# Kernel tuning notes

Hardware: AMD Instinct MI355X
Metric: run time of the kernel (lower is better)

## Reference

```python
import jax, jax.numpy as jnp
import numpy as np

DEPTH, DIM, HEADS, DH, MLP, N, B = 6, 192, 12, 16, 768, 256, 32
INNER = HEADS * DH  # 192


def setup_inputs() -> dict:
    key = jax.random.key(0)
    ks = jax.random.split(key, 10)
    w = lambda i, shape: jax.random.normal(ks[i], shape, dtype=jnp.float32) * 0.02
    return {
        'x': jax.random.normal(ks[0], (B, N, DIM), dtype=jnp.float32),
        'ln1_g': jnp.ones((DEPTH, DIM), jnp.float32),
        'ln1_b': jnp.zeros((DEPTH, DIM), jnp.float32),
        'Wq': w(1, (DEPTH, DIM, INNER)),
        'Wkv': w(2, (DEPTH, DIM, 2 * INNER)),
        'lsa_scale': jnp.full((DEPTH, HEADS), DH ** -0.5, dtype=jnp.float32),
        'mix_pre': jax.random.normal(ks[3], (DEPTH, HEADS, HEADS), dtype=jnp.float32),
        'mix_post': jax.random.normal(ks[4], (DEPTH, HEADS, HEADS), dtype=jnp.float32),
        'Wo': w(5, (DEPTH, INNER, DIM)),
        'bo': jnp.zeros((DEPTH, DIM), jnp.float32),
        'ls1': jnp.full((DEPTH, DIM), 0.1, dtype=jnp.float32),
        'ln2_g': jnp.ones((DEPTH, DIM), jnp.float32),
        'ln2_b': jnp.zeros((DEPTH, DIM), jnp.float32),
        'W1': w(6, (DEPTH, DIM, MLP)),
        'b1': jnp.zeros((DEPTH, MLP), jnp.float32),
        'W2': w(7, (DEPTH, MLP, DIM)),
        'b2': jnp.zeros((DEPTH, DIM), jnp.float32),
        'ls2': jnp.full((DEPTH, DIM), 0.1, dtype=jnp.float32),
    }


def _ln(x, g, b, eps=1e-5):
    m = x.mean(-1, keepdims=True)
    v = ((x - m) ** 2).mean(-1, keepdims=True)
    return (x - m) * jax.lax.rsqrt(v + eps) * g + b


def _heads(t, b, n):
    # (b, n, h*d) -> (b, h, n, d)
    return t.reshape(b, n, HEADS, DH).transpose(0, 2, 1, 3)


def _forward(x, ln1_g, ln1_b, Wq, Wkv, lsa_scale, mix_pre, mix_post, Wo, bo,
             ls1, ln2_g, ln2_b, W1, b1, W2, b2, ls2):
    b, n, _ = x.shape
    diag = jnp.arange(n)
    for l in range(DEPTH):
        # --- PreNorm + talking-heads LSA attention + LayerScale(0.1) ---
        h = _ln(x, ln1_g[l], ln1_b[l])
        q = _heads(h @ Wq[l], b, n)
        k, v = jnp.split(h @ Wkv[l], 2, axis=-1)
        k, v = _heads(k, b, n), _heads(v, b, n)
        dots = jnp.einsum('bhid,bhjd->bhij', q, k) * lsa_scale[l][None, :, None, None]
        # LSA: source sets diagonal to -1e-09 (literal, near-zero) when if_patch_attn
        dots = dots.at[:, :, diag, diag].set(-1e-9)
        dots = jnp.einsum('bhij,hg->bgij', dots, mix_pre[l])
        a = jax.nn.softmax(dots, axis=-1)
        a = jnp.einsum('bhij,hg->bgij', a, mix_post[l])
        o = jnp.einsum('bhij,bhjd->bhid', a, v)
        o = o.transpose(0, 2, 1, 3).reshape(b, n, INNER) @ Wo[l] + bo[l]
        x = x + o * ls1[l]
        # --- PreNorm + GELU FFN + LayerScale(0.1) ---
        h2 = _ln(x, ln2_g[l], ln2_b[l])
        f = jax.nn.gelu(h2 @ W1[l] + b1[l], approximate=False) @ W2[l] + b2[l]
        x = x + f * ls2[l]
    return x


def reference(x, ln1_g, ln1_b, Wq, Wkv, lsa_scale, mix_pre, mix_post, Wo, bo,
              ls1, ln2_g, ln2_b, W1, b1, W2, b2, ls2):
    return _forward(x, ln1_g, ln1_b, Wq, Wkv, lsa_scale, mix_pre, mix_post, Wo,
                    bo, ls1, ln2_g, ln2_b, W1, b1, W2, b2, ls2)
```

## Files before the change

kernel.cpp:

```cpp
#include <hip/hip_runtime.h>
#include <hip/hip_bf16.h>

#define DEPTH   6
#define DIM     192
#define HEADS   12
#define DH      16
#define MLPD    768
#define SEQ     256
#define BATCH   32
#define ROWS    (BATCH*SEQ)

typedef __attribute__((ext_vector_type(8))) short short8;
typedef __attribute__((ext_vector_type(4))) float f32x4;
typedef __attribute__((ext_vector_type(4))) _Float16 half4;
typedef __hip_bfloat16 bf16_t;
typedef _Float16 f16_t;

__device__ __forceinline__ bf16_t f2b(float v){ return __float2bfloat16(v); }
__device__ __forceinline__ ushort f2u(float v){
    union{ bf16_t b; ushort u; } w; w.b = __float2bfloat16(v); return w.u;
}
__device__ __forceinline__ f16_t u2h(ushort u){ union{ ushort u; f16_t h; } w; w.u = u; return w.h; }
__device__ __forceinline__ ushort h2u(f16_t h){ union{ ushort u; f16_t h; } w; w.h = h; return w.u; }

__device__ __forceinline__ void async16(ushort* lds, const ushort* gp){
    __builtin_amdgcn_global_load_lds(
        (const __attribute__((address_space(1))) uint*)gp,
        (__attribute__((address_space(3))) uint*)lds, 16, 0, 0);
}

__global__ void copy_kernel(const float* __restrict__ x, float* __restrict__ xr, int n){
    int i = blockIdx.x*256 + threadIdx.x;
    if (i < n) xr[i] = x[i];
}

__device__ __forceinline__ void wt_tile(const float* __restrict__ W,
        ushort* __restrict__ WT, int K, int N, int l, int tx, int ty,
        int tid, ushort* T){
    const float* src = W + ((size_t)l*K + tx*64)*N + ty*64;
    ushort* dst = WT + ((size_t)l*N + ty*64)*K + tx*64;
    int r = tid >> 2, c4 = (tid & 3)*16;
    #pragma unroll
    for (int u=0; u<4; u++){
        float4 v = *(const float4*)(src + (size_t)r*N + c4 + u*4);
        T[(c4+u*4+0)*72 + r] = f2u(v.x);
        T[(c4+u*4+1)*72 + r] = f2u(v.y);
        T[(c4+u*4+2)*72 + r] = f2u(v.z);
        T[(c4+u*4+3)*72 + r] = f2u(v.w);
    }
    __syncthreads();
    int n = tid >> 2, k8 = (tid & 3)*16;
    #pragma unroll
    for (int u=0; u<2; u++)
        *(uint4*)(dst + (size_t)n*K + k8 + u*8) = *(uint4*)&T[n*72 + k8 + u*8];
}

__global__ __launch_bounds__(256) void wt_all(
        const float* __restrict__ Wq, const float* __restrict__ Wkv,
        const float* __restrict__ Wo, const float* __restrict__ W1,
        const float* __restrict__ W2,
        ushort* __restrict__ WqT, ushort* __restrict__ WkvT,
        ushort* __restrict__ WoT, ushort* __restrict__ W1T,
        ushort* __restrict__ W2T){
    __shared__ ushort T[64*72];
    int id = blockIdx.x, l = blockIdx.y, tid = threadIdx.x;
    if (id < 9)       wt_tile(Wq,  WqT,  192, 192, l, id/3,       id%3,       tid, T);
    else if (id < 27) wt_tile(Wkv, WkvT, 192, 384, l, (id-9)/6,   (id-9)%6,   tid, T);
    else if (id < 36) wt_tile(Wo,  WoT,  192, 192, l, (id-27)/3,  (id-27)%3,  tid, T);
    else if (id < 72) wt_tile(W1,  W1T,  192, 768, l, (id-36)/12, (id-36)%12, tid, T);
    else              wt_tile(W2,  W2T,  768, 192, l, (id-72)/3,  (id-72)%3,  tid, T);
}

template<int MODE, int NT>
__global__ __launch_bounds__(256) void gemm_ln_kernel(
        const float* __restrict__ xres, const float* __restrict__ ln_g,
        const float* __restrict__ ln_b, const ushort* __restrict__ BT0,
        const ushort* __restrict__ BT1, const float* __restrict__ bias,
        f16_t* __restrict__ out0, f16_t* __restrict__ out1){
    __shared__ ushort As[64*200];
    __shared__ ushort Bs[2][6*2048];
    int tid = threadIdx.x, lane = tid & 63, w = tid >> 6;
    int bm = blockIdx.x*64;
    int tile0 = blockIdx.y*NT;
    auto issueB = [&](int t, int buf){
        int bn = (tile0 + t)*64;
        const ushort* bt; int bnl;
        if (MODE == 0 && bn >= DIM){ bt = BT1; bnl = bn - DIM; }
        else { bt = BT0; bnl = bn; }
        const ushort* bp = bt + (size_t)(bnl + (tid>>2))*DIM + (tid&3)*8;
        #pragma unroll
        for (int c=0; c<6; c++)
            async16(&Bs[buf][c*2048 + tid*8], bp + c*32);
    };
    issueB(0, 0);
    float g0 = ln_g[lane], g1 = ln_g[lane+64], g2 = ln_g[lane+128];
    float e0 = ln_b[lane], e1 = ln_b[lane+64], e2 = ln_b[lane+128];
    for (int it = 0; it < 16; it++){
        int r = (w<<4) + it;
        const float* xr = xres + (size_t)(bm + r)*DIM;
        float v0 = xr[lane], v1 = xr[lane+64], v2 = xr[lane+128];
        float s = v0+v1+v2;
        #pragma unroll
        for (int off=32; off; off>>=1) s += __shfl_xor(s, off, 64);
        float m = s*(1.0f/192.0f);
        float d0=v0-m, d1=v1-m, d2=v2-m;
        float q = d0*d0+d1*d1+d2*d2;
        #pragma unroll
        for (int off=32; off; off>>=1) q += __shfl_xor(q, off, 64);
        float inv = rsqrtf(q*(1.0f/192.0f) + 1e-5f);
        ushort* dst = &As[r*200];
        dst[lane]     = f2u(d0*inv*g0 + e0);
        dst[lane+64]  = f2u(d1*inv*g1 + e1);
        dst[lane+128] = f2u(d2*inv*g2 + e2);
    }
    __syncthreads();
    int wrow = w >> 1, wcol = w & 1;
    int quad = lane >> 4, mr = lane & 15;
    for (int t = 0; t < NT; t++){
        if (t+1 < NT) issueB(t+1, (t+1)&1);
        const ushort* B = Bs[t&1];
        f32x4 acc[2][2] = {};
        #pragma unroll
        for (int c = 0; c < 6; c++){
            short8 a0 = *(const short8*)&As[(wrow*32+mr)*200    + c*32 + quad*8];
            short8 a1 = *(const short8*)&As[(wrow*32+16+mr)*200 + c*32 + quad*8];
            short8 b0 = *(const short8*)&B[c*2048 + (wcol*32+mr)*32    + quad*8];
            short8 b1 = *(const short8*)&B[c*2048 + (wcol*32+16+mr)*32 + quad*8];
            acc[0][0] = __builtin_amdgcn_mfma_f32_16x16x32_bf16(a0, b0, acc[0][0], 0,0,0);
            acc[0][1] = __builtin_amdgcn_mfma_f32_16x16x32_bf16(a0, b1, acc[0][1], 0,0,0);
            acc[1][0] = __builtin_amdgcn_mfma_f32_16x16x32_bf16(a1, b0, acc[1][0], 0,0,0);
            acc[1][1] = __builtin_amdgcn_mfma_f32_16x16x32_bf16(a1, b1, acc[1][1], 0,0,0);
        }
        int bn = (tile0 + t)*64;
        #pragma unroll
        for (int rr=0; rr<2; rr++){
            #pragma unroll
            for (int cc=0; cc<2; cc++){
                int col = bn + wcol*32 + cc*16 + mr;
                if (MODE == 0){
                    f16_t* op; size_t st;
                    if (col < DIM){ op = out0 + col; st = DIM; }
                    else          { op = out1 + (col - DIM); st = 2*DIM; }
                    #pragma unroll
                    for (int tt=0; tt<4; tt++){
                        int row = bm + wrow*32 + rr*16 + quad*4 + tt;
                        op[(size_t)row*st] = (f16_t)acc[rr][cc][tt];
                    }
                } else {
                    float bv = bias[col];
                    #pragma unroll
                    for (int tt=0; tt<4; tt++){
                        int row = bm + wrow*32 + rr*16 + quad*4 + tt;
                        float z = acc[rr][cc][tt] + bv;
                        ((bf16_t*)out0)[(size_t)row*MLPD + col] =
                            f2b(0.5f*z*(1.0f + erff(z*0.70710678118654752f)));
                    }
                }
            }
        }
        __syncthreads();
    }
}

template<int ROUNDS>
__global__ __launch_bounds__(256) void gemm_a_kernel(
        const ushort* __restrict__ A, const ushort* __restrict__ BT,
        const float* __restrict__ bias, const float* __restrict__ ls,
        float* __restrict__ xres){
    const int K = ROUNDS*192;
    __shared__ ushort As[6*2048];
    __shared__ ushort Bs[6*2048];
    int tid = threadIdx.x, lane = tid & 63, w = tid >> 6;
    int wrow = w >> 1, wcol = w & 1;
    int bm = blockIdx.x*64, bn = blockIdx.y*64;
    int quad = lane >> 4, mr = lane & 15;
    const ushort* ap = A  + (size_t)(bm + (tid>>2))*K + (tid&3)*8;
    const ushort* bp = BT + (size_t)(bn + (tid>>2))*K + (tid&3)*8;
    f32x4 acc[2][2] = {};
    for (int r = 0; r < ROUNDS; r++){
        #pragma unroll
        for (int c=0; c<6; c++){
            async16(&As[c*2048 + tid*8], ap + r*192 + c*32);
            async16(&Bs[c*2048 + tid*8], bp + r*192 + c*32);
        }
        __syncthreads();
        #pragma unroll
        for (int c=0; c<6; c++){
            short8 a0 = *(const short8*)&As[c*2048 + (wrow*32+mr)*32    + quad*8];
            short8 a1 = *(const short8*)&As[c*2048 + (wrow*32+16+mr)*32 + quad*8];
            short8 b0 = *(const short8*)&Bs[c*2048 + (wcol*32+mr)*32    + quad*8];
            short8 b1 = *(const short8*)&Bs[c*2048 + (wcol*32+16+mr)*32 + quad*8];
            acc[0][0] = __builtin_amdgcn_mfma_f32_16x16x32_bf16(a0, b0, acc[0][0], 0,0,0);
            acc[0][1] = __builtin_amdgcn_mfma_f32_16x16x32_bf16(a0, b1, acc[0][1], 0,0,0);
            acc[1][0] = __builtin_amdgcn_mfma_f32_16x16x32_bf16(a1, b0, acc[1][0], 0,0,0);
            acc[1][1] = __builtin_amdgcn_mfma_f32_16x16x32_bf16(a1, b1, acc[1][1], 0,0,0);
        }
        if (r+1 < ROUNDS) __syncthreads();
    }
    #pragma unroll
    for (int rr=0; rr<2; rr++){
        #pragma unroll
        for (int cc=0; cc<2; cc++){
            int col = bn + wcol*32 + cc*16 + mr;
            float bv = bias[col], lv = ls[col];
            #pragma unroll
            for (int tt=0; tt<4; tt++){
                int row = bm + wrow*32 + rr*16 + quad*4 + tt;
                xres[(size_t)row*DIM + col] += (acc[rr][cc][tt] + bv)*lv;
            }
        }
    }
}

#define SLAB    4488
#define IST     280
#define KV_OFF  53856
#define ROWP    200
#define Q_OFF   66656
#define POST_OFF 70112
#define LTOT    71776

__global__ __launch_bounds__(1024, 1) void attn_kernel(
        const f16_t* __restrict__ qb, const f16_t* __restrict__ kvb,
        const float* __restrict__ lsa, const float* __restrict__ pre,
        const float* __restrict__ post, const ushort* __restrict__ WoT,
        const float* __restrict__ bo, const float* __restrict__ ls1,
        float* __restrict__ xres){
    __shared__ ushort L[LTOT];
    int tid  = threadIdx.x;
    int lane = tid & 63, w = tid >> 6;
    int quad = lane >> 4, nr = lane & 15;
    int b  = blockIdx.x >> 4;
    int i0 = (blockIdx.x & 15) << 4;

    {
        uint* Z = (uint*)&L[KV_OFF];
        for (int k = tid; k < (LTOT - KV_OFF)/2; k += 1024) Z[k] = 0;
    }
    __syncthreads();

    if (tid < 384){
        int e = tid*8, i = e/DIM, d = e%DIM, hh = d >> 4;
        float sc = lsa[hh];
        union { uint4 v; f16_t h[8]; } iv, ov;
        iv.v = *(const uint4*)(qb + (size_t)(b*SEQ + i0 + i)*DIM + d);
        #pragma unroll
        for (int u=0; u<8; u++) ov.h[u] = (f16_t)((float)iv.h[u]*sc);
        *(uint4*)&L[Q_OFF + i*ROWP + d] = ov.v;
    } else if (tid < 512){
        for (int k = tid-384; k < 256; k += 128){
            int gg = k >> 4, hh = k & 15;
            if (gg < 12 && hh < 12)
                L[POST_OFF + k] = h2u((f16_t)post[hh*12+gg]);
        }
    }
    auto stage_kv = [&](int c, int coloff){
        for (int u = tid; u < 1536; u += 1024){
            int e = u*8;
            int j = e/DIM, d = e%DIM;
            uint4 v = *(const uint4*)(kvb + (size_t)(b*SEQ + c*64 + j)*(2*DIM) + coloff + d);
            *(uint4*)&L[KV_OFF + j*ROWP + d] = v;
        }
    };
    __syncthreads();

    half4 qf[12];
    #pragma unroll
    for (int h=0; h<12; h++)
        qf[h] = *(const half4*)&L[Q_OFF + nr*ROWP + h*16 + quad*4];
    half4 postTf = *(const half4*)&L[POST_OFF + nr*16 + quad*4];

    {
        int jg = w*16 + nr;
        const f16_t* krow = kvb + (size_t)(b*SEQ + jg)*(2*DIM);
        f32x4 acc[12];
        #pragma unroll
        for (int h=0; h<12; h++){
            half4 bv = *(const half4*)(krow + h*DH + quad*4);
            acc[h] = __builtin_amdgcn_mfma_f32_16x16x16f16(qf[h], bv, (f32x4){0,0,0,0}, 0,0,0);
        }
        #pragma unroll
        for (int t=0; t<4; t++){
            if (i0 + quad*4 + t == jg){
                #pragma unroll
                for (int h=0; h<12; h++) acc[h][t] = -1e-9f;
            }
        }
        #pragma unroll
        for (int g=0; g<12; g++){
            float s0=0.f, s1=0.f, s2=0.f, s3=0.f;
            #pragma unroll
            for (int h=0; h<12; h++){
                float p = pre[h*12+g];
                s0 += acc[h][0]*p; s1 += acc[h][1]*p;
                s2 += acc[h][2]*p; s3 += acc[h][3]*p;
            }
            ushort* sp = &L[g*SLAB + jg];
            sp[(quad*4+0)*IST] = h2u((f16_t)s0);
            sp[(quad*4+1)*IST] = h2u((f16_t)s1);
            sp[(quad*4+2)*IST] = h2u((f16_t)s2);
            sp[(quad*4+3)*IST] = h2u((f16_t)s3);
        }
    }
    __syncthreads();

    for (int r = w; r < 192; r += 16){
        int g = r >> 4, i = r & 15;
        ushort* sp = &L[g*SLAB + i*IST];
        ushort4 uv = *(ushort4*)&sp[lane*4];
        float e0 = __expf((float)u2h(uv.x));
        float e1 = __expf((float)u2h(uv.y));
        float e2 = __expf((float)u2h(uv.z));
        float e3 = __expf((float)u2h(uv.w));
        float ssum = e0+e1+e2+e3;
        #pragma unroll
        for (int off=32; off; off>>=1) ssum += __shfl_xor(ssum, off, 64);
        float rin = 1.0f/ssum;
        uv.x = h2u((f16_t)(e0*rin)); uv.y = h2u((f16_t)(e1*rin));
        uv.z = h2u((f16_t)(e2*rin)); uv.w = h2u((f16_t)(e3*rin));
        *(ushort4*)&sp[lane*4] = uv;
    }
    __syncthreads();

    for (int s = 0; s < 16; s++){
        int cb = s*16 + w;
        int i = cb >> 4, jb = cb & 15;
        int colbase = i*IST + jb*16 + nr;
        half4 bv;
        #pragma unroll
        for (int t=0; t<4; t++) bv[t] = u2h(L[(quad*4+t)*SLAB + colbase]);
        f32x4 cc = __builtin_amdgcn_mfma_f32_16x16x16f16(postTf, bv, (f32x4){0,0,0,0}, 0,0,0);
        if (quad < 3){
            #pragma unroll
            for (int t=0; t<4; t++) L[(quad*4+t)*SLAB + colbase] = h2u((f16_t)cc[t]);
        }
    }
    __syncthreads();

    f32x4 oacc = {0,0,0,0};
    for (int c = 0; c < 4; c++){
        stage_kv(c, DIM);
        __syncthreads();
        if (w < 12){
            int g = w;
            #pragma unroll
            for (int ks = 0; ks < 4; ks++){
                int jl = ks*16 + quad*4;
                half4 av = *(const half4*)&L[g*SLAB + nr*IST + c*64 + jl];
                half4 bv;
                #pragma unroll
                for (int t=0; t<4; t++) bv[t] = u2h(L[KV_OFF + (jl+t)*ROWP + g*16 + nr]);
                oacc = __builtin_amdgcn_mfma_f32_16x16x16f16(av, bv, oacc, 0,0,0);
            }
        }
        __syncthreads();
    }

    {
        for (int u = tid; u < 4608; u += 1024){
            int e = u*8;
            int c = e/12288, rem = e - c*12288;
            int n = rem >> 6, kk = rem & 63;
            async16(&L[e], WoT + (size_t)n*192 + c*64 + kk);
        }
        if (w < 12){
            int g = w;
            #pragma unroll
            for (int t=0; t<4; t++){
                int i = quad*4 + t;
                L[Q_OFF + i*ROWP + g*16 + nr] = f2u(oacc[t]);
            }
        }
    }
    __syncthreads();

    if (w < 12){
        f32x4 wacc = {0,0,0,0};
        int ct = w;
        #pragma unroll
        for (int c = 0; c < 3; c++){
            #pragma unroll
            for (int sub = 0; sub < 2; sub++){
                int k0 = c*64 + sub*32;
                short8 av = *(const short8*)&L[Q_OFF + nr*ROWP + k0 + quad*8];
                short8 bv = *(const short8*)&L[c*12288 + (ct*16 + nr)*64 + sub*32 + quad*8];
                wacc = __builtin_amdgcn_mfma_f32_16x16x32_bf16(av, bv, wacc, 0,0,0);
            }
        }
        int col = ct*16 + nr;
        float bv2 = bo[col], lv = ls1[col];
        #pragma unroll
        for (int t=0; t<4; t++){
            int row = b*SEQ + i0 + quad*4 + t;
            xres[(size_t)row*DIM + col] += (wacc[t] + bv2)*lv;
        }
    }
}

extern "C" void kernel_launch(void* const* d_in, const int* in_sizes, int n_in,
                              void* d_out, int out_size, void* d_ws, size_t ws_size,
                              hipStream_t stream){
    const float* x    = (const float*)d_in[0];
    const float* ln1g = (const float*)d_in[1];
    const float* ln1b = (const float*)d_in[2];
    const float* Wq   = (const float*)d_in[3];
    const float* Wkv  = (const float*)d_in[4];
    const float* lsa  = (const float*)d_in[5];
    const float* pre  = (const float*)d_in[6];
    const float* post = (const float*)d_in[7];
    const float* Wo   = (const float*)d_in[8];
    const float* bo   = (const float*)d_in[9];
    const float* ls1  = (const float*)d_in[10];
    const float* ln2g = (const float*)d_in[11];
    const float* ln2b = (const float*)d_in[12];
    const float* W1   = (const float*)d_in[13];
    const float* b1   = (const float*)d_in[14];
    const float* W2   = (const float*)d_in[15];
    const float* b2   = (const float*)d_in[16];
    const float* ls2  = (const float*)d_in[17];
    float* xres = (float*)d_out;

    char* ws = (char*)d_ws;
    f16_t*  qb  = (f16_t*)ws;
    f16_t*  kvb = (f16_t*)(ws + (size_t)ROWS*DIM*2);
    bf16_t* fb  = (bf16_t*)ws;
    char* p = ws + (size_t)ROWS*MLPD*2;
    ushort* WqT  = (ushort*)p; p += (size_t)DEPTH*DIM*DIM*2;
    ushort* WkvT = (ushort*)p; p += (size_t)DEPTH*DIM*2*DIM*2;
    ushort* WoT  = (ushort*)p; p += (size_t)DEPTH*DIM*DIM*2;
    ushort* W1T  = (ushort*)p; p += (size_t)DEPTH*DIM*MLPD*2;
    ushort* W2T  = (ushort*)p; p += (size_t)DEPTH*MLPD*DIM*2;

    int ntot = ROWS*DIM;
    copy_kernel<<<ntot/256, 256, 0, stream>>>(x, xres, ntot);
    wt_all<<<dim3(108, 6), 256, 0, stream>>>(Wq, Wkv, Wo, W1, W2,
                                             WqT, WkvT, WoT, W1T, W2T);
    for (int l = 0; l < DEPTH; l++){
        gemm_ln_kernel<0,3><<<dim3(128,3), 256, 0, stream>>>(xres,
                ln1g + l*DIM, ln1b + l*DIM,
                WqT + (size_t)l*DIM*DIM, WkvT + (size_t)l*DIM*2*DIM,
                nullptr, qb, kvb);
        attn_kernel<<<BATCH*(SEQ/16), 1024, 0, stream>>>(qb, kvb, lsa + l*HEADS,
                pre + l*HEADS*HEADS, post + l*HEADS*HEADS,
                WoT + (size_t)l*DIM*DIM, bo + l*DIM, ls1 + l*DIM, xres);
        gemm_ln_kernel<1,4><<<dim3(128,3), 256, 0, stream>>>(xres,
                ln2g + l*DIM, ln2b + l*DIM,
                W1T + (size_t)l*DIM*MLPD, nullptr, b1 + l*MLPD, (f16_t*)fb, nullptr);
        gemm_a_kernel<4><<<dim3(128,3), 256, 0, stream>>>((const ushort*)fb,
                W2T + (size_t)l*MLPD*DIM, b2 + l*DIM, ls2 + l*DIM, xres);
    }
}
```

Before: 708.0 us.

## Double-buffer V staging via idle warps and retune attention LDS layout

The attention kernel now double-buffers the V chunks. Warps 12-15, which sit idle during the P·V MFMAs, prefetch the next 64-row chunk while warps 0-11 compute, so the staging load and its sync no longer sit on the critical path between steps. It also changes LDS strides and padding (IST, KVR) to alter bank patterns, and remaps block indices to spread batches across blocks. Smaller edits: it drops a barrier after the zero-fill, folds the diagonal mask into the score store, uses packed f32x2 math for the head mixing, and partially unrolls the softmax and post-mix loops. The diagonal is now written as zero instead of -1e-9, which matches after the f16 cast, and LDS usage grows.

```diff
diff --git a/kernel.cpp b/kernel.cpp
--- a/kernel.cpp
+++ b/kernel.cpp
@@ -12,6 +12,7 @@
 
 typedef __attribute__((ext_vector_type(8))) short short8;
 typedef __attribute__((ext_vector_type(4))) float f32x4;
+typedef __attribute__((ext_vector_type(2))) float f32x2;
 typedef __attribute__((ext_vector_type(4))) _Float16 half4;
 typedef __hip_bfloat16 bf16_t;
 typedef _Float16 f16_t;
@@ -212,13 +213,16 @@
     }
 }
 
-#define SLAB    4488
-#define IST     280
-#define KV_OFF  53856
-#define ROWP    200
-#define Q_OFF   66656
-#define POST_OFF 70112
-#define LTOT    71776
+#define IST      260
+#define SLAB     4168
+#define KV0      50016
+#define KVR      216
+#define KVSZ     13824
+#define KV1      (KV0+KVSZ)
+#define Q_OFF    77664
+#define ROWP     200
+#define POST_OFF 80864
+#define LTOT     81120
 
 __global__ __launch_bounds__(1024, 1) void attn_kernel(
         const f16_t* __restrict__ qb, const f16_t* __restrict__ kvb,
@@ -230,15 +234,15 @@
     int tid  = threadIdx.x;
     int lane = tid & 63, w = tid >> 6;
     int quad = lane >> 4, nr = lane & 15;
-    int b  = blockIdx.x >> 4;
-    int i0 = (blockIdx.x & 15) << 4;
+    int bid = blockIdx.x;
+    int qq  = bid >> 3;
+    int b   = (bid & 7)*4 + (qq >> 4);
+    int i0  = (qq & 15) << 4;
 
     {
-        uint* Z = (uint*)&L[KV_OFF];
-        for (int k = tid; k < (LTOT - KV_OFF)/2; k += 1024) Z[k] = 0;
-    }
-    __syncthreads();
-
+        uint* Z = (uint*)&L[KV0];
+        for (int k = tid; k < (16*SLAB - KV0)/2; k += 1024) Z[k] = 0;
+    }
     if (tid < 384){
         int e = tid*8, i = e/DIM, d = e%DIM, hh = d >> 4;
         float sc = lsa[hh];
@@ -250,18 +254,10 @@
     } else if (tid < 512){
         for (int k = tid-384; k < 256; k += 128){
             int gg = k >> 4, hh = k & 15;
-            if (gg < 12 && hh < 12)
-                L[POST_OFF + k] = h2u((f16_t)post[hh*12+gg]);
-        }
-    }
-    auto stage_kv = [&](int c, int coloff){
-        for (int u = tid; u < 1536; u += 1024){
-            int e = u*8;
-            int j = e/DIM, d = e%DIM;
-            uint4 v = *(const uint4*)(kvb + (size_t)(b*SEQ + c*64 + j)*(2*DIM) + coloff + d);
-            *(uint4*)&L[KV_OFF + j*ROWP + d] = v;
-        }
-    };
+            L[POST_OFF + k] = (gg < 12 && hh < 12) ? h2u((f16_t)post[hh*12+gg])
+                                                   : (ushort)0;
+        }
+    }
     __syncthreads();
 
     half4 qf[12];
@@ -279,31 +275,29 @@
             half4 bv = *(const half4*)(krow + h*DH + quad*4);
             acc[h] = __builtin_amdgcn_mfma_f32_16x16x16f16(qf[h], bv, (f32x4){0,0,0,0}, 0,0,0);
         }
-        #pragma unroll
-        for (int t=0; t<4; t++){
-            if (i0 + quad*4 + t == jg){
-                #pragma unroll
-                for (int h=0; h<12; h++) acc[h][t] = -1e-9f;
-            }
-        }
+        int dd = jg - (i0 + quad*4);
         #pragma unroll
         for (int g=0; g<12; g++){
-            float s0=0.f, s1=0.f, s2=0.f, s3=0.f;
+            f32x2 s01 = {0.f, 0.f}, s23 = {0.f, 0.f};
             #pragma unroll
             for (int h=0; h<12; h++){
                 float p = pre[h*12+g];
-                s0 += acc[h][0]*p; s1 += acc[h][1]*p;
-                s2 += acc[h][2]*p; s3 += acc[h][3]*p;
+                f32x2 pp  = {p, p};
+                f32x2 a01 = {acc[h][0], acc[h][1]};
+                f32x2 a23 = {acc[h][2], acc[h][3]};
+                s01 += a01*pp;
+                s23 += a23*pp;
             }
             ushort* sp = &L[g*SLAB + jg];
-            sp[(quad*4+0)*IST] = h2u((f16_t)s0);
-            sp[(quad*4+1)*IST] = h2u((f16_t)s1);
-            sp[(quad*4+2)*IST] = h2u((f16_t)s2);
-            sp[(quad*4+3)*IST] = h2u((f16_t)s3);
-        }
-    }
-    __syncthreads();
-
+            sp[(quad*4+0)*IST] = (dd==0) ? (ushort)0 : h2u((f16_t)s01.x);
+            sp[(quad*4+1)*IST] = (dd==1) ? (ushort)0 : h2u((f16_t)s01.y);
+            sp[(quad*4+2)*IST] = (dd==2) ? (ushort)0 : h2u((f16_t)s23.x);
+            sp[(quad*4+3)*IST] = (dd==3) ? (ushort)0 : h2u((f16_t)s23.y);
+        }
+    }
+    __syncthreads();
+
+    #pragma unroll 2
     for (int r = w; r < 192; r += 16){
         int g = r >> 4, i = r & 15;
         ushort* sp = &L[g*SLAB + i*IST];
@@ -322,6 +316,7 @@
     }
     __syncthreads();
 
+    #pragma unroll 2
     for (int s = 0; s < 16; s++){
         int cb = s*16 + w;
         int i = cb >> 4, jb = cb & 15;
@@ -337,21 +332,32 @@
     }
     __syncthreads();
 
+    auto stage_chunk = [&](int c, int buf, int id, int step){
+        ushort* dst = &L[KV0 + buf*KVSZ];
+        for (int u = id; u < 1536; u += step){
+            int e = u*8, j = e/192, d = e - j*192;
+            uint4 v = *(const uint4*)(kvb + (size_t)(b*SEQ + c*64 + j)*(2*DIM) + DIM + d);
+            *(uint4*)&dst[j*KVR + d] = v;
+        }
+    };
     f32x4 oacc = {0,0,0,0};
+    stage_chunk(0, 0, tid, 1024);
+    __syncthreads();
     for (int c = 0; c < 4; c++){
-        stage_kv(c, DIM);
-        __syncthreads();
         if (w < 12){
-            int g = w;
+            const int g = w;
+            const ushort* Vb = &L[KV0 + (c&1)*KVSZ];
             #pragma unroll
             for (int ks = 0; ks < 4; ks++){
                 int jl = ks*16 + quad*4;
                 half4 av = *(const half4*)&L[g*SLAB + nr*IST + c*64 + jl];
                 half4 bv;
                 #pragma unroll
-                for (int t=0; t<4; t++) bv[t] = u2h(L[KV_OFF + (jl+t)*ROWP + g*16 + nr]);
+                for (int t=0; t<4; t++) bv[t] = u2h(Vb[(jl+t)*KVR + g*16 + nr]);
                 oacc = __builtin_amdgcn_mfma_f32_16x16x16f16(av, bv, oacc, 0,0,0);
             }
+        } else if (c+1 < 4){
+            stage_chunk(c+1, (c+1)&1, tid-768, 256);
         }
         __syncthreads();
     }
```

Result: slower. 821.5 us (+16.0%).

## Fold pre-softmax head mixing into QK MFMA and read Wo directly from global

Applied to the files above, without the earlier changes.

Instead of computing twelve per-head QK scores and then mixing them with the pre matrix in scalar FMAs, each output head's mixed scores are computed directly by scaling the Q fragments by pre coefficients and running six 16x16x32 MFMAs over the full 192-wide inner dimension. This moves the head-mixing arithmetic onto the matrix units at the cost of more MFMA calls. The pre matrix is staged in LDS as fp16, and the diagonal is written as zero rather than -1e-9 after mixing. The Wo projection also drops its LDS staging via async loads and reads B fragments straight from global memory.

```diff
diff --git a/kernel.cpp b/kernel.cpp
--- a/kernel.cpp
+++ b/kernel.cpp
@@ -13,6 +13,7 @@
 typedef __attribute__((ext_vector_type(8))) short short8;
 typedef __attribute__((ext_vector_type(4))) float f32x4;
 typedef __attribute__((ext_vector_type(4))) _Float16 half4;
+typedef __attribute__((ext_vector_type(8))) _Float16 half8;
 typedef __hip_bfloat16 bf16_t;
 typedef _Float16 f16_t;
 
@@ -218,7 +219,8 @@
 #define ROWP    200
 #define Q_OFF   66656
 #define POST_OFF 70112
-#define LTOT    71776
+#define PRE_OFF 71776
+#define LTOT    71920
 
 __global__ __launch_bounds__(1024, 1) void attn_kernel(
         const f16_t* __restrict__ qb, const f16_t* __restrict__ kvb,
@@ -253,6 +255,9 @@
             if (gg < 12 && hh < 12)
                 L[POST_OFF + k] = h2u((f16_t)post[hh*12+gg]);
         }
+    } else if (tid < 640){
+        for (int k = tid-512; k < 144; k += 128)
+            L[PRE_OFF + k] = h2u((f16_t)pre[k]);
     }
     auto stage_kv = [&](int c, int coloff){
         for (int u = tid; u < 1536; u += 1024){
@@ -264,42 +269,34 @@
     };
     __syncthreads();
 
-    half4 qf[12];
-    #pragma unroll
-    for (int h=0; h<12; h++)
-        qf[h] = *(const half4*)&L[Q_OFF + nr*ROWP + h*16 + quad*4];
     half4 postTf = *(const half4*)&L[POST_OFF + nr*16 + quad*4];
 
     {
         int jg = w*16 + nr;
         const f16_t* krow = kvb + (size_t)(b*SEQ + jg)*(2*DIM);
-        f32x4 acc[12];
-        #pragma unroll
-        for (int h=0; h<12; h++){
-            half4 bv = *(const half4*)(krow + h*DH + quad*4);
-            acc[h] = __builtin_amdgcn_mfma_f32_16x16x16f16(qf[h], bv, (f32x4){0,0,0,0}, 0,0,0);
-        }
-        #pragma unroll
-        for (int t=0; t<4; t++){
-            if (i0 + quad*4 + t == jg){
-                #pragma unroll
-                for (int h=0; h<12; h++) acc[h][t] = -1e-9f;
-            }
-        }
+        half8 qh[6], kh[6];
+        #pragma unroll
+        for (int c=0; c<6; c++){
+            union{ short8 s; half8 h; } a, k2;
+            a.s  = *(const short8*)&L[Q_OFF + nr*ROWP + c*32 + quad*8];
+            k2.s = *(const short8*)(const void*)(krow + c*32 + quad*8);
+            qh[c] = a.h; kh[c] = k2.h;
+        }
+        int dd = jg - (i0 + quad*4);
+        int hb = (quad>>1)*12;
         #pragma unroll
         for (int g=0; g<12; g++){
-            float s0=0.f, s1=0.f, s2=0.f, s3=0.f;
-            #pragma unroll
-            for (int h=0; h<12; h++){
-                float p = pre[h*12+g];
-                s0 += acc[h][0]*p; s1 += acc[h][1]*p;
-                s2 += acc[h][2]*p; s3 += acc[h][3]*p;
+            f32x4 a = {0,0,0,0};
+            #pragma unroll
+            for (int c=0; c<6; c++){
+                f16_t s = u2h(L[PRE_OFF + hb + c*24 + g]);
+                a = __builtin_amdgcn_mfma_f32_16x16x32_f16(qh[c]*s, kh[c], a, 0,0,0);
             }
             ushort* sp = &L[g*SLAB + jg];
-            sp[(quad*4+0)*IST] = h2u((f16_t)s0);
-            sp[(quad*4+1)*IST] = h2u((f16_t)s1);
-            sp[(quad*4+2)*IST] = h2u((f16_t)s2);
-            sp[(quad*4+3)*IST] = h2u((f16_t)s3);
+            sp[(quad*4+0)*IST] = (dd==0) ? (ushort)0 : h2u((f16_t)a[0]);
+            sp[(quad*4+1)*IST] = (dd==1) ? (ushort)0 : h2u((f16_t)a[1]);
+            sp[(quad*4+2)*IST] = (dd==2) ? (ushort)0 : h2u((f16_t)a[2]);
+            sp[(quad*4+3)*IST] = (dd==3) ? (ushort)0 : h2u((f16_t)a[3]);
         }
     }
     __syncthreads();
@@ -356,20 +353,12 @@
         __syncthreads();
     }
 
-    {
-        for (int u = tid; u < 4608; u += 1024){
-            int e = u*8;
-            int c = e/12288, rem = e - c*12288;
-            int n = rem >> 6, kk = rem & 63;
-            async16(&L[e], WoT + (size_t)n*192 + c*64 + kk);
-        }
-        if (w < 12){
-            int g = w;
-            #pragma unroll
-            for (int t=0; t<4; t++){
-                int i = quad*4 + t;
-                L[Q_OFF + i*ROWP + g*16 + nr] = f2u(oacc[t]);
-            }
+    if (w < 12){
+        int g = w;
+        #pragma unroll
+        for (int t=0; t<4; t++){
+            int i = quad*4 + t;
+            L[Q_OFF + i*ROWP + g*16 + nr] = f2u(oacc[t]);
         }
     }
     __syncthreads();
@@ -377,13 +366,14 @@
     if (w < 12){
         f32x4 wacc = {0,0,0,0};
         int ct = w;
+        const ushort* wg = WoT + (size_t)(ct*16 + nr)*192;
         #pragma unroll
         for (int c = 0; c < 3; c++){
             #pragma unroll
             for (int sub = 0; sub < 2; sub++){
                 int k0 = c*64 + sub*32;
                 short8 av = *(const short8*)&L[Q_OFF + nr*ROWP + k0 + quad*8];
-                short8 bv = *(const short8*)&L[c*12288 + (ct*16 + nr)*64 + sub*32 + quad*8];
+                short8 bv = *(const short8*)(wg + k0 + quad*8);
                 wacc = __builtin_amdgcn_mfma_f32_16x16x32_bf16(av, bv, wacc, 0,0,0);
             }
         }
```

Result: no change. 703.9 us (-0.6%).
